# Optimization experiments

Hardware: AMD Instinct MI355X
Metric: run time of the kernel (lower is better)

## Reference

```python
import jax, jax.numpy as jnp
import numpy as np

B, S, D_IN, HID, H = 4, 2048, 1024, 1024, 16
DH = HID // H


def setup_inputs() -> dict:
    key = jax.random.key(0)
    ks = jax.random.split(key, 10)
    s = 0.02
    return {
        "x": jax.random.normal(ks[0], (B, S, D_IN), dtype=jnp.float32),
        "Wq": jax.random.normal(ks[1], (D_IN, HID), dtype=jnp.float32) * s,
        "bq": jnp.zeros((HID,), dtype=jnp.float32),
        "Wk": jax.random.normal(ks[2], (D_IN, HID), dtype=jnp.float32) * s,
        "bk": jnp.zeros((HID,), dtype=jnp.float32),
        "Wv": jax.random.normal(ks[3], (D_IN, HID), dtype=jnp.float32) * s,
        "bv": jnp.zeros((HID,), dtype=jnp.float32),
        "Wo": jax.random.normal(ks[4], (HID, HID), dtype=jnp.float32) * s,
        "bo": jnp.zeros((HID,), dtype=jnp.float32),
        "padding_mask": jax.random.randint(ks[5], (B, S), 0, 2, dtype=jnp.int32),
    }


def reference(x, Wq, bq, Wk, bk, Wv, bv, Wo, bo, padding_mask):
    b, s, _ = x.shape
    q = (x @ Wq + bq).reshape(b, s, H, DH)  # [b, s, h, dh]
    k = (x @ Wk + bk).reshape(b, s, H, DH)
    v = (x @ Wv + bv).reshape(b, s, H, DH)

    # ALiBi: symmetric |i-j| distance bias, per-head slopes 2^{-m}
    r = jnp.arange(s)
    pos = jnp.abs(r[None, :] - r[:, None]).astype(jnp.float32)  # [s, s]
    step = 8.0 / H
    slopes = jnp.power(2.0, -jnp.arange(step, 8.0 + step, step, dtype=jnp.float32))  # [h]
    alibi = slopes[:, None, None] * pos[None, :, :]  # [h, s, s]

    scale = jnp.sqrt(jnp.float32(DH))
    attn = jnp.einsum("bqhd,bkhd->bhqk", q, k)
    attn = (attn - alibi[None]) / scale
    attn = jnp.where(padding_mask[:, None, None, :] == 0, -jnp.inf, attn)
    p = jax.nn.softmax(attn, axis=-1)

    out = jnp.einsum("bhqk,bkhd->bqhd", p, v).reshape(b, s, HID)
    return out @ Wo + bo
```

## Files before the change

### kernel.cpp

```cpp
#include <hip/hip_runtime.h>
#include <stdint.h>

#define NB     4
#define SEQ    2048
#define NH     16
#define DHD    64
#define DM     1024
#define MTOT   (NB*SEQ)

typedef __attribute__((ext_vector_type(8))) short bf16x8;
typedef __attribute__((ext_vector_type(4))) float f32x4;

__device__ __forceinline__ short f2bf(float f) {
  uint32_t u = __float_as_uint(f);
  u = (u + 0x7FFFu + ((u >> 16) & 1u)) >> 16;
  return (short)u;
}

__device__ __forceinline__ uint32_t cvtpk(float lo, float hi) {
  uint32_t r;
  asm("v_cvt_pk_bf16_f32 %0, %1, %2" : "=v"(r) : "v"(lo), "v"(hi));
  return r;
}

__device__ __forceinline__ float exp2a(float x) {
  float r;
  asm("v_exp_f32 %0, %1" : "=v"(r) : "v"(x));
  return r;
}

__device__ __forceinline__ float max3f(float a, float b, float c) {
  return fmaxf(fmaxf(a, b), c);
}

__device__ __forceinline__ f32x4 mfma16(bf16x8 a, bf16x8 b, f32x4 c) {
  return __builtin_amdgcn_mfma_f32_16x16x32_bf16(a, b, c, 0, 0, 0);
}

__device__ __forceinline__ void async16(const void* g, void* l) {
  __builtin_amdgcn_global_load_lds(
      (const __attribute__((address_space(1))) void*)g,
      (__attribute__((address_space(3))) void*)l, 16, 0, 0);
}

__global__ void k_cast(const float* __restrict__ in, short* __restrict__ out, int n) {
  int i = (blockIdx.x * blockDim.x + threadIdx.x) * 8;
  if (i >= n) return;
  float4 a = *reinterpret_cast<const float4*>(in + i);
  float4 b = *reinterpret_cast<const float4*>(in + i + 4);
  bf16x8 v;
  v[0] = f2bf(a.x); v[1] = f2bf(a.y); v[2] = f2bf(a.z); v[3] = f2bf(a.w);
  v[4] = f2bf(b.x); v[5] = f2bf(b.y); v[6] = f2bf(b.z); v[7] = f2bf(b.w);
  *reinterpret_cast<bf16x8*>(out + i) = v;
}

__global__ void k_maskbias(const int* __restrict__ pm, float* __restrict__ fb, int n) {
  int i = blockIdx.x * blockDim.x + threadIdx.x;
  if (i < n) fb[i] = pm[i] ? 0.0f : -1e30f;
}

__global__ void k_transpose(const float* __restrict__ in, short* __restrict__ out) {
  __shared__ float tile[32][33];
  int n0 = blockIdx.x * 32, k0 = blockIdx.y * 32;
  int tx = threadIdx.x, ty = threadIdx.y;
  #pragma unroll
  for (int i = 0; i < 32; i += 8)
    tile[ty + i][tx] = in[(size_t)(k0 + ty + i) * DM + n0 + tx];
  __syncthreads();
  #pragma unroll
  for (int i = 0; i < 32; i += 8)
    out[(size_t)(n0 + ty + i) * DM + k0 + tx] = f2bf(tile[tx][ty + i]);
}

template<int MODE>
__global__ void __launch_bounds__(256) k_gemm(const short* __restrict__ A,
                                              const short* __restrict__ Bt,
                                              const float* __restrict__ bias,
                                              void* __restrict__ Cv, float scale) {
  __shared__ short lA[128 * 32];
  __shared__ short lB[128 * 32];
  int lin = blockIdx.y * gridDim.x + blockIdx.x;
  int s = ((lin & 7) << 6) | (lin >> 3);
  int m0 = (s & 63) * 128, n0 = (s >> 6) * 128;
  int tid = threadIdx.x, lane = tid & 63, w = tid >> 6;
  int wr = w >> 1, wc = w & 1;
  int l15 = lane & 15, lg = lane >> 4;
  f32x4 acc[4][4] = {};

  int r0 = tid >> 2, c0 = (tid & 3) * 8;
  int r1 = (tid + 256) >> 2, c1 = ((tid + 256) & 3) * 8;
  const short* ga0 = A + (size_t)(m0 + r0) * DM + c0;
  const short* ga1 = A + (size_t)(m0 + r1) * DM + c1;
  const short* gb0 = Bt + (size_t)(n0 + r0) * DM + c0;
  const short* gb1 = Bt + (size_t)(n0 + r1) * DM + c1;
  short* lA0 = lA + w * 512;
  short* lA1 = lA + 2048 + w * 512;
  short* lB0 = lB + w * 512;
  short* lB1 = lB + 2048 + w * 512;

  for (int k0 = 0; k0 < DM; k0 += 32) {
    async16(ga0 + k0, lA0);
    async16(ga1 + k0, lA1);
    async16(gb0 + k0, lB0);
    async16(gb1 + k0, lB1);
    __syncthreads();
    bf16x8 af[4], bfr[4];
    #pragma unroll
    for (int i = 0; i < 4; ++i) {
      af[i]  = *reinterpret_cast<const bf16x8*>(lA + (wr * 64 + i * 16 + l15) * 32 + lg * 8);
      bfr[i] = *reinterpret_cast<const bf16x8*>(lB + (wc * 64 + i * 16 + l15) * 32 + lg * 8);
    }
    #pragma unroll
    for (int i = 0; i < 4; ++i)
      #pragma unroll
      for (int j = 0; j < 4; ++j)
        acc[i][j] = mfma16(af[i], bfr[j], acc[i][j]);
    __syncthreads();
  }

  #pragma unroll
  for (int j = 0; j < 4; ++j) {
    int cg = n0 + wc * 64 + j * 16 + l15;
    float bv = bias[cg];
    #pragma unroll
    for (int i = 0; i < 4; ++i) {
      #pragma unroll
      for (int r = 0; r < 4; ++r) {
        int rg = m0 + wr * 64 + i * 16 + lg * 4 + r;
        float val = (acc[i][j][r] + bv) * scale;
        if (MODE == 0)
          ((short*)Cv)[(size_t)rg * DM + cg] = f2bf(val);
        else if (MODE == 1)
          ((short*)Cv)[((size_t)((rg >> 11) * DM + cg)) * SEQ + (rg & 2047)] = f2bf(val);
        else
          ((float*)Cv)[(size_t)rg * DM + cg] = val;
      }
    }
  }
}

__global__ void __launch_bounds__(256) k_attn(const short* __restrict__ Q,
                                              const short* __restrict__ Kb,
                                              const short* __restrict__ Vt,
                                              const float* __restrict__ fbias,
                                              short* __restrict__ O) {
  __shared__ short lK[2][64 * 64];
  __shared__ short lV[2][64 * 64];
  __shared__ uint32_t pbuf[4 * 16 * 36];
  int qt = blockIdx.x, bh = blockIdx.y;
  int b = bh >> 4, h = bh & 15;
  int tid = threadIdx.x, lane = tid & 63, w = tid >> 6;
  int l15 = lane & 15, lg = lane >> 4;
  int q0 = qt * 64 + w * 16;
  float c2 = exp2f(-0.5f * (float)(h + 1)) * 0.125f * 1.44269504f;

  const short* qp = Q + (size_t)(b * SEQ + q0 + l15) * DM + h * DHD + lg * 8;
  bf16x8 bq0 = *reinterpret_cast<const bf16x8*>(qp);
  bf16x8 bq1 = *reinterpret_cast<const bf16x8*>(qp + 32);

  int srow0 = w * 8 + (lane >> 3);
  int srow1 = srow0 + 32;
  int sc0 = (lane & 7) ^ (srow0 & 7);
  int sc1 = (lane & 7) ^ (srow1 & 7);
  const short* kg0 = Kb + (size_t)(b * SEQ + srow0) * DM + h * DHD + sc0 * 8;
  const short* kg1 = Kb + (size_t)(b * SEQ + srow1) * DM + h * DHD + sc1 * 8;
  const short* vg0 = Vt + ((size_t)bh * DHD + srow0) * SEQ + sc0 * 8;
  const short* vg1 = Vt + ((size_t)bh * DHD + srow1) * SEQ + sc1 * 8;

  const float* fb = fbias + b * SEQ;
  uint32_t* wb = pbuf + w * 576 + l15 * 36;
  int sw = l15 & 7;

  float mrun = -1e30f, ssum = 0.0f;
  f32x4 acc[4] = {};
  float d0 = (float)(q0 + l15) - (float)(lg * 4);

  async16(kg0, &lK[0][w * 512]);
  async16(kg1, &lK[0][2048 + w * 512]);
  async16(vg0, &lV[0][w * 512]);
  async16(vg1, &lV[0][2048 + w * 512]);
  kg0 += (size_t)64 * DM; kg1 += (size_t)64 * DM; vg0 += 64; vg1 += 64;
  asm volatile("s_waitcnt vmcnt(0)" ::: "memory");
  __builtin_amdgcn_s_barrier();
  __builtin_amdgcn_sched_barrier(0);

  for (int kt = 0; kt < SEQ; kt += 64) {
    int cur = (kt >> 6) & 1;
    const short* Kc = lK[cur];
    const short* Vc = lV[cur];

    float4 fb4[4];
    #pragma unroll
    for (int t = 0; t < 4; ++t)
      fb4[t] = *reinterpret_cast<const float4*>(fb + kt + t * 16 + lg * 4);
    __builtin_amdgcn_sched_barrier(0);

    if (kt + 64 < SEQ) {
      short* nK = (short*)lK[cur ^ 1];
      short* nV = (short*)lV[cur ^ 1];
      async16(kg0, nK + w * 512);
      async16(kg1, nK + 2048 + w * 512);
      async16(vg0, nV + w * 512);
      async16(vg1, nV + 2048 + w * 512);
      kg0 += (size_t)64 * DM; kg1 += (size_t)64 * DM; vg0 += 64; vg1 += 64;
    }

    f32x4 st[4];
    __builtin_amdgcn_s_setprio(1);
    #pragma unroll
    for (int t = 0; t < 4; ++t) {
      int row = t * 16 + l15;
      bf16x8 k0 = *reinterpret_cast<const bf16x8*>(Kc + row * 64 + (lg ^ sw) * 8);
      bf16x8 k1 = *reinterpret_cast<const bf16x8*>(Kc + row * 64 + ((lg + 4) ^ sw) * 8);
      f32x4 z = {};
      z = mfma16(k0, bq0, z);
      st[t] = mfma16(k1, bq1, z);
    }
    __builtin_amdgcn_s_setprio(0);

    float l[4][4];
    #pragma unroll
    for (int t = 0; t < 4; ++t) {
      l[t][0] = fmaf(-c2, fabsf(d0 - (float)(t * 16 + 0)), st[t][0] + fb4[t].x);
      l[t][1] = fmaf(-c2, fabsf(d0 - (float)(t * 16 + 1)), st[t][1] + fb4[t].y);
      l[t][2] = fmaf(-c2, fabsf(d0 - (float)(t * 16 + 2)), st[t][2] + fb4[t].z);
      l[t][3] = fmaf(-c2, fabsf(d0 - (float)(t * 16 + 3)), st[t][3] + fb4[t].w);
    }

    float ma = max3f(l[0][0], l[0][1], l[0][2]);
    float mb = max3f(l[0][3], l[1][0], l[1][1]);
    float mc = max3f(l[1][2], l[1][3], l[2][0]);
    float md = max3f(l[2][1], l[2][2], l[2][3]);
    float me = max3f(l[3][0], l[3][1], l[3][2]);
    float tmax = fmaxf(max3f(ma, mb, mc), max3f(md, me, l[3][3]));
    tmax = fmaxf(tmax, __shfl_xor(tmax, 16));
    tmax = fmaxf(tmax, __shfl_xor(tmax, 32));

    if (!__all(tmax <= mrun + 8.0f)) {
      float mn = fmaxf(mrun, tmax);
      float fsc = exp2a(mrun - mn);
      mrun = mn;
      ssum *= fsc;
      #pragma unroll
      for (int td = 0; td < 4; ++td) acc[td] *= fsc;
    }

    float p[16];
    #pragma unroll
    for (int t = 0; t < 4; ++t)
      #pragma unroll
      for (int r = 0; r < 4; ++r)
        p[t * 4 + r] = exp2a(l[t][r] - mrun);
    float a0 = p[0] + p[1],  a1 = p[2] + p[3],  a2 = p[4] + p[5],  a3 = p[6] + p[7];
    float a4 = p[8] + p[9],  a5 = p[10] + p[11], a6 = p[12] + p[13], a7 = p[14] + p[15];
    float b0 = a0 + a1, b1 = a2 + a3, b2 = a4 + a5, b3 = a6 + a7;
    float rs = (b0 + b1) + (b2 + b3);
    rs += __shfl_xor(rs, 16);
    rs += __shfl_xor(rs, 32);
    ssum += rs;

    #pragma unroll
    for (int t = 0; t < 4; ++t) {
      uint2 wv = { cvtpk(p[t * 4 + 0], p[t * 4 + 1]), cvtpk(p[t * 4 + 2], p[t * 4 + 3]) };
      *reinterpret_cast<uint2*>(wb + t * 8 + lg * 2) = wv;
    }
    asm volatile("s_waitcnt lgkmcnt(0)" ::: "memory");
    __builtin_amdgcn_sched_barrier(0);

    __builtin_amdgcn_s_setprio(1);
    #pragma unroll
    for (int ks = 0; ks < 2; ++ks) {
      int t = ks * 2 + (lg >> 1);
      bf16x8 pf = *reinterpret_cast<const bf16x8*>(wb + t * 8 + (lg & 1) * 4);
      #pragma unroll
      for (int td = 0; td < 4; ++td) {
        int row = td * 16 + l15;
        bf16x8 vf = *reinterpret_cast<const bf16x8*>(Vc + row * 64 + ((ks * 4 + lg) ^ sw) * 8);
        acc[td] = mfma16(vf, pf, acc[td]);
      }
    }
    __builtin_amdgcn_s_setprio(0);
    d0 -= 64.0f;

    asm volatile("s_waitcnt vmcnt(0)" ::: "memory");
    __builtin_amdgcn_s_barrier();
    __builtin_amdgcn_sched_barrier(0);
  }

  float inv = 1.0f / ssum;
  short* op = O + (size_t)(b * SEQ + q0 + l15) * DM + h * DHD;
  #pragma unroll
  for (int td = 0; td < 4; ++td) {
    uint2 wv = { cvtpk(acc[td][0] * inv, acc[td][1] * inv),
                 cvtpk(acc[td][2] * inv, acc[td][3] * inv) };
    *reinterpret_cast<uint2*>(op + td * 16 + lg * 4) = wv;
  }
}

extern "C" void kernel_launch(void* const* d_in, const int* in_sizes, int n_in,
                              void* d_out, int out_size, void* d_ws, size_t ws_size,
                              hipStream_t stream) {
  const float* x  = (const float*)d_in[0];
  const float* Wq = (const float*)d_in[1];
  const float* bq = (const float*)d_in[2];
  const float* Wk = (const float*)d_in[3];
  const float* bk = (const float*)d_in[4];
  const float* Wv = (const float*)d_in[5];
  const float* bv = (const float*)d_in[6];
  const float* Wo = (const float*)d_in[7];
  const float* bo = (const float*)d_in[8];
  const int*   pm = (const int*)d_in[9];

  char* ws = (char*)d_ws;
  const size_t MB = 1ull << 20;
  short* xb  = (short*)(ws + 0 * MB);
  short* q   = (short*)(ws + 16 * MB);
  short* k   = (short*)(ws + 32 * MB);
  short* vt  = (short*)(ws + 48 * MB);
  short* ob  = (short*)(ws + 64 * MB);
  short* wqt = (short*)(ws + 80 * MB);
  short* wkt = (short*)(ws + 82 * MB);
  short* wvt = (short*)(ws + 84 * MB);
  short* wot = (short*)(ws + 86 * MB);
  float* fbias = (float*)(ws + 88 * MB);

  k_cast<<<dim3(MTOT * DM / 8 / 256), dim3(256), 0, stream>>>(x, xb, MTOT * DM);
  k_maskbias<<<dim3(MTOT / 256), dim3(256), 0, stream>>>(pm, fbias, MTOT);
  k_transpose<<<dim3(32, 32), dim3(32, 8), 0, stream>>>(Wq, wqt);
  k_transpose<<<dim3(32, 32), dim3(32, 8), 0, stream>>>(Wk, wkt);
  k_transpose<<<dim3(32, 32), dim3(32, 8), 0, stream>>>(Wv, wvt);
  k_transpose<<<dim3(32, 32), dim3(32, 8), 0, stream>>>(Wo, wot);
  k_gemm<0><<<dim3(64, 8), dim3(256), 0, stream>>>(xb, wqt, bq, q, 0.125f * 1.44269504f);
  k_gemm<0><<<dim3(64, 8), dim3(256), 0, stream>>>(xb, wkt, bk, k, 1.0f);
  k_gemm<1><<<dim3(64, 8), dim3(256), 0, stream>>>(xb, wvt, bv, vt, 1.0f);
  k_attn<<<dim3(SEQ / 64, NB * NH), dim3(256), 0, stream>>>(q, k, vt, fbias, ob);
  k_gemm<2><<<dim3(64, 8), dim3(256), 0, stream>>>(ob, wot, bo, d_out, 1.0f);
}
```

Measured before the change: 295.2 us.

## Process two query sub-tiles per wave and single-buffer K/V in attention

Each wave now handles 32 query rows as two 16-row halves that share every K and V fragment read from LDS, doubling MFMA work per LDS load and halving the grid. K/V shared memory drops from double to single buffering, with loads issued at the top of each iteration and guarded by __syncthreads, and launch bounds now request 4 blocks per CU. This trades the previous prefetch overlap for better reuse and occupancy. It risks exposing global load latency and raising register pressure from two sets of accumulators.

```diff
diff --git a/kernel.cpp b/kernel.cpp
--- a/kernel.cpp
+++ b/kernel.cpp
@@ -139,24 +139,75 @@
   }
 }
 
-__global__ void __launch_bounds__(256) k_attn(const short* __restrict__ Q,
-                                              const short* __restrict__ Kb,
-                                              const short* __restrict__ Vt,
-                                              const float* __restrict__ fbias,
-                                              short* __restrict__ O) {
-  __shared__ short lK[2][64 * 64];
-  __shared__ short lV[2][64 * 64];
-  __shared__ uint32_t pbuf[4 * 16 * 36];
+__device__ __forceinline__ void softmax_half(const f32x4* st, const float4* fb4,
+                                             float c2, float d0, int lg,
+                                             float& mrun, float& ssum,
+                                             f32x4* acc, uint32_t* wb) {
+  float l[16];
+  #pragma unroll
+  for (int t = 0; t < 4; ++t) {
+    l[t * 4 + 0] = fmaf(-c2, fabsf(d0 - (float)(t * 16 + 0)), st[t][0] + fb4[t].x);
+    l[t * 4 + 1] = fmaf(-c2, fabsf(d0 - (float)(t * 16 + 1)), st[t][1] + fb4[t].y);
+    l[t * 4 + 2] = fmaf(-c2, fabsf(d0 - (float)(t * 16 + 2)), st[t][2] + fb4[t].z);
+    l[t * 4 + 3] = fmaf(-c2, fabsf(d0 - (float)(t * 16 + 3)), st[t][3] + fb4[t].w);
+  }
+  float ma = max3f(l[0], l[1], l[2]);
+  float mb = max3f(l[3], l[4], l[5]);
+  float mc = max3f(l[6], l[7], l[8]);
+  float md = max3f(l[9], l[10], l[11]);
+  float me = max3f(l[12], l[13], l[14]);
+  float tmax = fmaxf(max3f(ma, mb, mc), max3f(md, me, l[15]));
+  tmax = fmaxf(tmax, __shfl_xor(tmax, 16));
+  tmax = fmaxf(tmax, __shfl_xor(tmax, 32));
+
+  if (!__all(tmax <= mrun + 8.0f)) {
+    float mn = fmaxf(mrun, tmax);
+    float fsc = exp2a(mrun - mn);
+    mrun = mn;
+    ssum *= fsc;
+    #pragma unroll
+    for (int td = 0; td < 4; ++td) acc[td] *= fsc;
+  }
+
+  float p[16];
+  #pragma unroll
+  for (int i = 0; i < 16; ++i) p[i] = exp2a(l[i] - mrun);
+  float a0 = p[0] + p[1],  a1 = p[2] + p[3],  a2 = p[4] + p[5],  a3 = p[6] + p[7];
+  float a4 = p[8] + p[9],  a5 = p[10] + p[11], a6 = p[12] + p[13], a7 = p[14] + p[15];
+  float b0 = a0 + a1, b1 = a2 + a3, b2 = a4 + a5, b3 = a6 + a7;
+  float rs = (b0 + b1) + (b2 + b3);
+  rs += __shfl_xor(rs, 16);
+  rs += __shfl_xor(rs, 32);
+  ssum += rs;
+
+  #pragma unroll
+  for (int t = 0; t < 4; ++t) {
+    uint2 wv = { cvtpk(p[t * 4 + 0], p[t * 4 + 1]), cvtpk(p[t * 4 + 2], p[t * 4 + 3]) };
+    *reinterpret_cast<uint2*>(wb + t * 8 + lg * 2) = wv;
+  }
+}
+
+__global__ void __launch_bounds__(256, 4) k_attn(const short* __restrict__ Q,
+                                                 const short* __restrict__ Kb,
+                                                 const short* __restrict__ Vt,
+                                                 const float* __restrict__ fbias,
+                                                 short* __restrict__ O) {
+  __shared__ short lK[64 * 64];
+  __shared__ short lV[64 * 64];
+  __shared__ uint32_t pbuf[4 * 2 * 16 * 36];
   int qt = blockIdx.x, bh = blockIdx.y;
   int b = bh >> 4, h = bh & 15;
   int tid = threadIdx.x, lane = tid & 63, w = tid >> 6;
   int l15 = lane & 15, lg = lane >> 4;
-  int q0 = qt * 64 + w * 16;
+  int q0 = qt * 128 + w * 32;
   float c2 = exp2f(-0.5f * (float)(h + 1)) * 0.125f * 1.44269504f;
 
-  const short* qp = Q + (size_t)(b * SEQ + q0 + l15) * DM + h * DHD + lg * 8;
-  bf16x8 bq0 = *reinterpret_cast<const bf16x8*>(qp);
-  bf16x8 bq1 = *reinterpret_cast<const bf16x8*>(qp + 32);
+  const short* qpA = Q + (size_t)(b * SEQ + q0 + l15) * DM + h * DHD + lg * 8;
+  bf16x8 bqA0 = *reinterpret_cast<const bf16x8*>(qpA);
+  bf16x8 bqA1 = *reinterpret_cast<const bf16x8*>(qpA + 32);
+  const short* qpB = qpA + (size_t)16 * DM;
+  bf16x8 bqB0 = *reinterpret_cast<const bf16x8*>(qpB);
+  bf16x8 bqB1 = *reinterpret_cast<const bf16x8*>(qpB + 32);
 
   int srow0 = w * 8 + (lane >> 3);
   int srow1 = srow0 + 32;
@@ -166,104 +217,54 @@
   const short* kg1 = Kb + (size_t)(b * SEQ + srow1) * DM + h * DHD + sc1 * 8;
   const short* vg0 = Vt + ((size_t)bh * DHD + srow0) * SEQ + sc0 * 8;
   const short* vg1 = Vt + ((size_t)bh * DHD + srow1) * SEQ + sc1 * 8;
+  short* dK0 = lK + w * 512;
+  short* dK1 = lK + 2048 + w * 512;
+  short* dV0 = lV + w * 512;
+  short* dV1 = lV + 2048 + w * 512;
 
   const float* fb = fbias + b * SEQ;
-  uint32_t* wb = pbuf + w * 576 + l15 * 36;
+  uint32_t* wbA = pbuf + w * 1152 + l15 * 36;
+  uint32_t* wbB = wbA + 576;
   int sw = l15 & 7;
 
-  float mrun = -1e30f, ssum = 0.0f;
-  f32x4 acc[4] = {};
-  float d0 = (float)(q0 + l15) - (float)(lg * 4);
-
-  async16(kg0, &lK[0][w * 512]);
-  async16(kg1, &lK[0][2048 + w * 512]);
-  async16(vg0, &lV[0][w * 512]);
-  async16(vg1, &lV[0][2048 + w * 512]);
-  kg0 += (size_t)64 * DM; kg1 += (size_t)64 * DM; vg0 += 64; vg1 += 64;
-  asm volatile("s_waitcnt vmcnt(0)" ::: "memory");
-  __builtin_amdgcn_s_barrier();
-  __builtin_amdgcn_sched_barrier(0);
+  float mrunA = -1e30f, ssumA = 0.0f, mrunB = -1e30f, ssumB = 0.0f;
+  f32x4 accA[4] = {}, accB[4] = {};
+  float d0A = (float)(q0 + l15) - (float)(lg * 4);
+  float d0B = d0A + 16.0f;
 
   for (int kt = 0; kt < SEQ; kt += 64) {
-    int cur = (kt >> 6) & 1;
-    const short* Kc = lK[cur];
-    const short* Vc = lV[cur];
+    async16(kg0, dK0);
+    async16(kg1, dK1);
+    async16(vg0, dV0);
+    async16(vg1, dV1);
+    kg0 += (size_t)64 * DM; kg1 += (size_t)64 * DM; vg0 += 64; vg1 += 64;
 
     float4 fb4[4];
     #pragma unroll
     for (int t = 0; t < 4; ++t)
       fb4[t] = *reinterpret_cast<const float4*>(fb + kt + t * 16 + lg * 4);
-    __builtin_amdgcn_sched_barrier(0);
-
-    if (kt + 64 < SEQ) {
-      short* nK = (short*)lK[cur ^ 1];
-      short* nV = (short*)lV[cur ^ 1];
-      async16(kg0, nK + w * 512);
-      async16(kg1, nK + 2048 + w * 512);
-      async16(vg0, nV + w * 512);
-      async16(vg1, nV + 2048 + w * 512);
-      kg0 += (size_t)64 * DM; kg1 += (size_t)64 * DM; vg0 += 64; vg1 += 64;
-    }
-
-    f32x4 st[4];
+
+    __syncthreads();
+
+    f32x4 stA[4], stB[4];
     __builtin_amdgcn_s_setprio(1);
     #pragma unroll
     for (int t = 0; t < 4; ++t) {
       int row = t * 16 + l15;
-      bf16x8 k0 = *reinterpret_cast<const bf16x8*>(Kc + row * 64 + (lg ^ sw) * 8);
-      bf16x8 k1 = *reinterpret_cast<const bf16x8*>(Kc + row * 64 + ((lg + 4) ^ sw) * 8);
-      f32x4 z = {};
-      z = mfma16(k0, bq0, z);
-      st[t] = mfma16(k1, bq1, z);
+      bf16x8 k0 = *reinterpret_cast<const bf16x8*>(lK + row * 64 + (lg ^ sw) * 8);
+      bf16x8 k1 = *reinterpret_cast<const bf16x8*>(lK + row * 64 + ((lg + 4) ^ sw) * 8);
+      f32x4 zA = {};
+      zA = mfma16(k0, bqA0, zA);
+      stA[t] = mfma16(k1, bqA1, zA);
+      f32x4 zB = {};
+      zB = mfma16(k0, bqB0, zB);
+      stB[t] = mfma16(k1, bqB1, zB);
     }
     __builtin_amdgcn_s_setprio(0);
 
-    float l[4][4];
-    #pragma unroll
-    for (int t = 0; t < 4; ++t) {
-      l[t][0] = fmaf(-c2, fabsf(d0 - (float)(t * 16 + 0)), st[t][0] + fb4[t].x);
-      l[t][1] = fmaf(-c2, fabsf(d0 - (float)(t * 16 + 1)), st[t][1] + fb4[t].y);
-      l[t][2] = fmaf(-c2, fabsf(d0 - (float)(t * 16 + 2)), st[t][2] + fb4[t].z);
-      l[t][3] = fmaf(-c2, fabsf(d0 - (float)(t * 16 + 3)), st[t][3] + fb4[t].w);
-    }
-
-    float ma = max3f(l[0][0], l[0][1], l[0][2]);
-    float mb = max3f(l[0][3], l[1][0], l[1][1]);
-    float mc = max3f(l[1][2], l[1][3], l[2][0]);
-    float md = max3f(l[2][1], l[2][2], l[2][3]);
-    float me = max3f(l[3][0], l[3][1], l[3][2]);
-    float tmax = fmaxf(max3f(ma, mb, mc), max3f(md, me, l[3][3]));
-    tmax = fmaxf(tmax, __shfl_xor(tmax, 16));
-    tmax = fmaxf(tmax, __shfl_xor(tmax, 32));
-
-    if (!__all(tmax <= mrun + 8.0f)) {
-      float mn = fmaxf(mrun, tmax);
-      float fsc = exp2a(mrun - mn);
-      mrun = mn;
-      ssum *= fsc;
-      #pragma unroll
-      for (int td = 0; td < 4; ++td) acc[td] *= fsc;
-    }
-
-    float p[16];
-    #pragma unroll
-    for (int t = 0; t < 4; ++t)
-      #pragma unroll
-      for (int r = 0; r < 4; ++r)
-        p[t * 4 + r] = exp2a(l[t][r] - mrun);
-    float a0 = p[0] + p[1],  a1 = p[2] + p[3],  a2 = p[4] + p[5],  a3 = p[6] + p[7];
-    float a4 = p[8] + p[9],  a5 = p[10] + p[11], a6 = p[12] + p[13], a7 = p[14] + p[15];
-    float b0 = a0 + a1, b1 = a2 + a3, b2 = a4 + a5, b3 = a6 + a7;
-    float rs = (b0 + b1) + (b2 + b3);
-    rs += __shfl_xor(rs, 16);
-    rs += __shfl_xor(rs, 32);
-    ssum += rs;
-
-    #pragma unroll
-    for (int t = 0; t < 4; ++t) {
-      uint2 wv = { cvtpk(p[t * 4 + 0], p[t * 4 + 1]), cvtpk(p[t * 4 + 2], p[t * 4 + 3]) };
-      *reinterpret_cast<uint2*>(wb + t * 8 + lg * 2) = wv;
-    }
+    softmax_half(stA, fb4, c2, d0A, lg, mrunA, ssumA, accA, wbA);
+    softmax_half(stB, fb4, c2, d0B, lg, mrunB, ssumB, accB, wbB);
+
     asm volatile("s_waitcnt lgkmcnt(0)" ::: "memory");
     __builtin_amdgcn_sched_barrier(0);
 
@@ -271,29 +272,33 @@
     #pragma unroll
     for (int ks = 0; ks < 2; ++ks) {
       int t = ks * 2 + (lg >> 1);
-      bf16x8 pf = *reinterpret_cast<const bf16x8*>(wb + t * 8 + (lg & 1) * 4);
+      bf16x8 pfA = *reinterpret_cast<const bf16x8*>(wbA + t * 8 + (lg & 1) * 4);
+      bf16x8 pfB = *reinterpret_cast<const bf16x8*>(wbB + t * 8 + (lg & 1) * 4);
       #pragma unroll
       for (int td = 0; td < 4; ++td) {
         int row = td * 16 + l15;
-        bf16x8 vf = *reinterpret_cast<const bf16x8*>(Vc + row * 64 + ((ks * 4 + lg) ^ sw) * 8);
-        acc[td] = mfma16(vf, pf, acc[td]);
+        bf16x8 vf = *reinterpret_cast<const bf16x8*>(lV + row * 64 + ((ks * 4 + lg) ^ sw) * 8);
+        accA[td] = mfma16(vf, pfA, accA[td]);
+        accB[td] = mfma16(vf, pfB, accB[td]);
       }
     }
     __builtin_amdgcn_s_setprio(0);
-    d0 -= 64.0f;
-
-    asm volatile("s_waitcnt vmcnt(0)" ::: "memory");
-    __builtin_amdgcn_s_barrier();
-    __builtin_amdgcn_sched_barrier(0);
-  }
-
-  float inv = 1.0f / ssum;
-  short* op = O + (size_t)(b * SEQ + q0 + l15) * DM + h * DHD;
+    d0A -= 64.0f; d0B -= 64.0f;
+    __syncthreads();
+  }
+
+  float invA = 1.0f / ssumA;
+  float invB = 1.0f / ssumB;
+  short* opA = O + (size_t)(b * SEQ + q0 + l15) * DM + h * DHD;
+  short* opB = opA + (size_t)16 * DM;
   #pragma unroll
   for (int td = 0; td < 4; ++td) {
-    uint2 wv = { cvtpk(acc[td][0] * inv, acc[td][1] * inv),
-                 cvtpk(acc[td][2] * inv, acc[td][3] * inv) };
-    *reinterpret_cast<uint2*>(op + td * 16 + lg * 4) = wv;
+    uint2 wvA = { cvtpk(accA[td][0] * invA, accA[td][1] * invA),
+                  cvtpk(accA[td][2] * invA, accA[td][3] * invA) };
+    *reinterpret_cast<uint2*>(opA + td * 16 + lg * 4) = wvA;
+    uint2 wvB = { cvtpk(accB[td][0] * invB, accB[td][1] * invB),
+                  cvtpk(accB[td][2] * invB, accB[td][3] * invB) };
+    *reinterpret_cast<uint2*>(opB + td * 16 + lg * 4) = wvB;
   }
 }
 
@@ -333,6 +338,6 @@
   k_gemm<0><<<dim3(64, 8), dim3(256), 0, stream>>>(xb, wqt, bq, q, 0.125f * 1.44269504f);
   k_gemm<0><<<dim3(64, 8), dim3(256), 0, stream>>>(xb, wkt, bk, k, 1.0f);
   k_gemm<1><<<dim3(64, 8), dim3(256), 0, stream>>>(xb, wvt, bv, vt, 1.0f);
-  k_attn<<<dim3(SEQ / 64, NB * NH), dim3(256), 0, stream>>>(q, k, vt, fbias, ob);
+  k_attn<<<dim3(SEQ / 128, NB * NH), dim3(256), 0, stream>>>(q, k, vt, fbias, ob);
   k_gemm<2><<<dim3(64, 8), dim3(256), 0, stream>>>(ob, wot, bo, d_out, 1.0f);
 }
```

New measurement: 283.9 us. 1.04x faster.
